# Performance work log

Hardware: AMD Instinct MI355X
Metric: run time of the kernel (lower is better)

Reference implementation:

```python
import jax, jax.numpy as jnp
import numpy as np

B, S, H, KVH, D = 1, 2048, 32, 8, 128
ROPE_THETA = 500000.0


def _rotate_half(x):
    x1, x2 = jnp.split(x, 2, axis=-1)
    return jnp.concatenate((-x2, x1), axis=-1)


def setup_inputs() -> dict:
    key = jax.random.key(0)
    ks = jax.random.split(key, 5)
    hidden_states = jax.random.normal(ks[0], (B, S, H * D), dtype=jnp.float32)
    Wq = jax.random.normal(ks[1], (H * D, H * D), dtype=jnp.float32) * 0.02
    Wk = jax.random.normal(ks[2], (KVH * D, H * D), dtype=jnp.float32) * 0.02
    Wv = jax.random.normal(ks[3], (KVH * D, H * D), dtype=jnp.float32) * 0.02
    Wo = jax.random.normal(ks[4], (H * D, H * D), dtype=jnp.float32) * 0.02
    # rotary tables (Llama-style, concat of freqs with itself)
    inv_freq = 1.0 / (ROPE_THETA ** (jnp.arange(0, D, 2, dtype=jnp.float32) / D))
    freqs = jnp.arange(S, dtype=jnp.float32)[:, None] * inv_freq[None, :]  # [S, D/2]
    emb = jnp.concatenate((freqs, freqs), axis=-1)  # [S, D]
    cos = jnp.cos(emb)[None]  # [1, S, D]
    sin = jnp.sin(emb)[None]
    # additive causal mask, matching SDPA attn_mask semantics
    causal = jnp.tril(jnp.ones((S, S), dtype=bool))
    attention_mask = jnp.where(causal, 0.0, -1e9).astype(jnp.float32)[None, None]  # [1,1,S,S]
    return {"hidden_states": hidden_states, "attention_mask": attention_mask,
            "cos": cos, "sin": sin, "Wq": Wq, "Wk": Wk, "Wv": Wv, "Wo": Wo}


def reference(hidden_states, attention_mask, cos, sin, Wq, Wk, Wv, Wo):
    b, s, _ = hidden_states.shape
    d = cos.shape[-1]
    h = Wq.shape[0] // d
    kvh = Wk.shape[0] // d
    g = h // kvh  # GQA group size

    # fused QKV projection (nn.Linear: y = x @ W^T), then split heads -> [b, heads, s, d]
    q = jnp.einsum('bsi,oi->bso', hidden_states, Wq).reshape(b, s, h, d).transpose(0, 2, 1, 3)
    k = jnp.einsum('bsi,oi->bso', hidden_states, Wk).reshape(b, s, kvh, d).transpose(0, 2, 1, 3)
    v = jnp.einsum('bsi,oi->bso', hidden_states, Wv).reshape(b, s, kvh, d).transpose(0, 2, 1, 3)

    # rotary embedding (unsqueeze_dim=1)
    c = cos[:, None]  # [b,1,s,d]
    sn = sin[:, None]
    q = q * c + _rotate_half(q) * sn
    k = k * c + _rotate_half(k) * sn

    # GQA: view q as [b, kvh, g, s, d]; contract against un-repeated k/v
    qg = q.reshape(b, kvh, g, s, d)
    scale = 1.0 / jnp.sqrt(jnp.float32(d))
    scores = jnp.einsum('bkgsd,bktd->bkgst', qg, k) * scale  # [b,kvh,g,s,s]
    scores = scores + attention_mask[:, :, None]  # broadcast [b,1,1,s,s]
    probs = jax.nn.softmax(scores, axis=-1)
    attn = jnp.einsum('bkgst,bktd->bkgsd', probs, v)  # [b,kvh,g,s,d]

    attn = attn.reshape(b, h, s, d).transpose(0, 2, 1, 3).reshape(b, s, h * d)
    out = jnp.einsum('bso,po->bsp', attn, Wo)
    return out
```

## Files before the change

### kernel.cpp

```cpp
#include <hip/hip_runtime.h>
#include <hip/hip_bf16.h>

#define SEQ 2048
#define HD  128
#define NH  32
#define NKV 8
#define MODEL 4096
#define KVDIM 1024
#define QKVN 6144

typedef __attribute__((ext_vector_type(8))) short short8;
typedef __attribute__((ext_vector_type(4))) short short4v;
typedef __attribute__((ext_vector_type(4))) float float4v;

#define MFMA16(a, b, c) __builtin_amdgcn_mfma_f32_16x16x32_bf16(a, b, c, 0, 0, 0)

__device__ __forceinline__ short f2bf(float x) {
  unsigned u = __builtin_bit_cast(unsigned, x);
  u += 0x7fffu + ((u >> 16) & 1u);
  return (short)(u >> 16);
}

__device__ __forceinline__ void async_copy16(const void* g, void* l) {
  __builtin_amdgcn_global_load_lds((const __attribute__((address_space(1))) void*)g,
                                   (__attribute__((address_space(3))) void*)l, 16, 0, 0);
}

__global__ __launch_bounds__(256) void cast_bf16(const float* __restrict__ in,
                                                 short* __restrict__ out, int n) {
  int i = (blockIdx.x * 256 + threadIdx.x) * 4;
  if (i < n) {
    float4v v = *(const float4v*)(in + i);
    short4v o;
    o[0] = f2bf(v[0]); o[1] = f2bf(v[1]); o[2] = f2bf(v[2]); o[3] = f2bf(v[3]);
    *(short4v*)(out + i) = o;
  }
}

#define BM 128
#define BN 128
#define BK 32

__global__ __launch_bounds__(256) void gemm_nt(const short* __restrict__ A,
                                               const short* __restrict__ B,
                                               float* __restrict__ C,
                                               int M, int N, int K) {
  __shared__ __align__(16) short As[2][BM * BK];
  __shared__ __align__(16) short Bs[2][BN * BK];
  int t = threadIdx.x;
  int w = t >> 6, lane = t & 63;
  int col = lane & 15, quad = lane >> 4;
  int m0 = blockIdx.y * BM, n0 = blockIdx.x * BN;
  int wr = (w >> 1) * 64, wc = (w & 1) * 64;

  int srow   = lane >> 2;
  int schunk = (lane & 3) ^ ((lane >> 3) & 3);
  const short* Ag0 = A + (size_t)(m0 + w * 32 + srow) * K + schunk * 8;
  const short* Ag1 = Ag0 + (size_t)16 * K;
  const short* Bg0 = B + (size_t)(n0 + w * 32 + srow) * K + schunk * 8;
  const short* Bg1 = Bg0 + (size_t)16 * K;
  const int wofs0 = (w * 32) * BK;
  const int wofs1 = (w * 32 + 16) * BK;

  int aswz = (quad ^ ((col >> 1) & 3)) * 8;

  float4v acc[4][4] = {};

  async_copy16(Ag0, &As[0][wofs0]);
  async_copy16(Ag1, &As[0][wofs1]);
  async_copy16(Bg0, &Bs[0][wofs0]);
  async_copy16(Bg1, &Bs[0][wofs1]);
  __syncthreads();

  const int iters = K / BK;
  for (int it = 0; it < iters; it++) {
    const int cb = it & 1, nb = cb ^ 1;
    if (it + 1 < iters) {
      const int k0 = (it + 1) * BK;
      async_copy16(Ag0 + k0, &As[nb][wofs0]);
      async_copy16(Ag1 + k0, &As[nb][wofs1]);
      async_copy16(Bg0 + k0, &Bs[nb][wofs0]);
      async_copy16(Bg1 + k0, &Bs[nb][wofs1]);
    }
    short8 af[4], bfr[4];
#pragma unroll
    for (int i = 0; i < 4; i++)
      af[i] = *(const short8*)&As[cb][(wr + i * 16 + col) * BK + aswz];
#pragma unroll
    for (int i = 0; i < 4; i++)
      bfr[i] = *(const short8*)&Bs[cb][(wc + i * 16 + col) * BK + aswz];
#pragma unroll
    for (int mi = 0; mi < 4; mi++)
#pragma unroll
      for (int ni = 0; ni < 4; ni++)
        acc[mi][ni] = MFMA16(af[mi], bfr[ni], acc[mi][ni]);
    __syncthreads();
  }

#pragma unroll
  for (int mi = 0; mi < 4; mi++)
#pragma unroll
    for (int ni = 0; ni < 4; ni++)
#pragma unroll
      for (int r = 0; r < 4; r++) {
        int row = m0 + wr + mi * 16 + quad * 4 + r;
        int cc  = n0 + wc + ni * 16 + col;
        C[(size_t)row * N + cc] = acc[mi][ni][r];
      }
}

__global__ __launch_bounds__(128) void rope_kernel(const float* __restrict__ qkv,
                                                   const float* __restrict__ cosp,
                                                   const float* __restrict__ sinp,
                                                   short* __restrict__ qb,
                                                   short* __restrict__ kb) {
  int s = blockIdx.x, head = blockIdx.y, d = threadIdx.x;
  float c  = cosp[s * HD + d];
  float sn = sinp[s * HD + d];
  if (head < NH) {
    const float* base = qkv + (size_t)s * QKVN + head * HD;
    float x = base[d];
    float rot = (d < 64) ? -base[d + 64] : base[d - 64];
    qb[((size_t)(head * SEQ + s)) * HD + d] = f2bf((x * c + rot * sn) * 0.08838834764831845f);
  } else {
    int hk = head - NH;
    const float* base = qkv + (size_t)s * QKVN + MODEL + hk * HD;
    float x = base[d];
    float rot = (d < 64) ? -base[d + 64] : base[d - 64];
    kb[((size_t)(hk * SEQ + s)) * HD + d] = f2bf(x * c + rot * sn);
  }
}

__global__ __launch_bounds__(256) void vtrans_kernel(const float* __restrict__ qkv,
                                                     short* __restrict__ vt) {
  __shared__ float tile[32][33];
  int kv = blockIdx.z;
  int d0 = blockIdx.x * 32, s0 = blockIdx.y * 32;
  int tx = threadIdx.x, ty = threadIdx.y;
#pragma unroll
  for (int j = 0; j < 32; j += 8)
    tile[ty + j][tx] = qkv[(size_t)(s0 + ty + j) * QKVN + MODEL + KVDIM + kv * HD + d0 + tx];
  __syncthreads();
#pragma unroll
  for (int j = 0; j < 32; j += 8)
    vt[((size_t)(kv * HD + d0 + ty + j)) * SEQ + s0 + tx] = f2bf(tile[tx][ty + j]);
}

#define FKT 32
#define KLD 136
#define VLD 40
#define PLD 40

__global__ __launch_bounds__(256, 3) void flash_attn(const short* __restrict__ qb_,
                                                     const short* __restrict__ kb,
                                                     const short* __restrict__ vt,
                                                     short* __restrict__ attn) {
  __shared__ __align__(16) short Ks[2][FKT * KLD];
  __shared__ __align__(16) short Vs[2][HD * VLD];
  __shared__ __align__(16) short Ps[4][32 * PLD];
  const int tid = threadIdx.x;
  const int w = tid >> 6, lane = tid & 63;
  const int col = lane & 15, quad = lane >> 4;
  const int h = blockIdx.x;
  const int kv = h >> 2;
  const int yp = (blockIdx.y < 8) ? (15 - (int)blockIdx.y) : ((int)blockIdx.y - 8);
  const int qB0 = yp * 128;
  const int q0w = qB0 + w * 32;
  const int ntiles = qB0 / FKT + 4;

  short8 ones;
#pragma unroll
  for (int i = 0; i < 8; i++) ones[i] = (short)0x3F80;

  short8 qf[2][4];
  const short* qbase = qb_ + ((size_t)(h * SEQ + q0w + col)) * HD;
#pragma unroll
  for (int rt = 0; rt < 2; rt++)
#pragma unroll
    for (int ks = 0; ks < 4; ks++)
      qf[rt][ks] = *(const short8*)(qbase + rt * 16 * HD + ks * 32 + quad * 8);

  float4v o[2][8] = {};
  float4v la[2] = {};

  const int kg_off = tid * 8;
  const int klds0  = (kg_off >> 7) * KLD + (kg_off & 127);
  const int vd     = tid >> 2;
  const int vkof   = (tid & 3) * 8;
  const size_t vrow0 = ((size_t)(kv * HD + vd)) * SEQ;
  const size_t vrow1 = ((size_t)(kv * HD + vd + 64)) * SEQ;
  const int vlds0 = vd * VLD + vkof;
  const short* kgbase = kb + ((size_t)kv * SEQ) * HD;

  short8 kr0, kr1, vr0, vr1;
  kr0 = *(const short8*)(kgbase + kg_off);
  kr1 = *(const short8*)(kgbase + 2048 + kg_off);
  vr0 = *(const short8*)(vt + vrow0 + vkof);
  vr1 = *(const short8*)(vt + vrow1 + vkof);
  *(short8*)&Ks[0][klds0]            = kr0;
  *(short8*)&Ks[0][klds0 + 16 * KLD] = kr1;
  *(short8*)&Vs[0][vlds0]            = vr0;
  *(short8*)&Vs[0][vlds0 + 64 * VLD] = vr1;
  __syncthreads();

  for (int kt = 0; kt < ntiles; kt++) {
    const int b = kt & 1;
    const int key0 = kt * FKT;
    if (kt + 1 < ntiles) {
      const int nk0 = key0 + FKT;
      const short* kg = kgbase + (size_t)nk0 * HD;
      kr0 = *(const short8*)(kg + kg_off);
      kr1 = *(const short8*)(kg + 2048 + kg_off);
      vr0 = *(const short8*)(vt + vrow0 + nk0 + vkof);
      vr1 = *(const short8*)(vt + vrow1 + nk0 + vkof);
    }
    if (key0 <= q0w + 31) {
      float4v sc[2][2] = {};
#pragma unroll
      for (int ks = 0; ks < 4; ks++) {
        short8 kf0 = *(const short8*)&Ks[b][col * KLD + ks * 32 + quad * 8];
        short8 kf1 = *(const short8*)&Ks[b][(16 + col) * KLD + ks * 32 + quad * 8];
        sc[0][0] = MFMA16(qf[0][ks], kf0, sc[0][0]);
        sc[0][1] = MFMA16(qf[0][ks], kf1, sc[0][1]);
        sc[1][0] = MFMA16(qf[1][ks], kf0, sc[1][0]);
        sc[1][1] = MFMA16(qf[1][ks], kf1, sc[1][1]);
      }
      short* pw = Ps[w];
#pragma unroll
      for (int rt = 0; rt < 2; rt++)
#pragma unroll
        for (int r = 0; r < 4; r++) {
          int row = q0w + rt * 16 + quad * 4 + r;
          float s0 = sc[rt][0][r]; if (key0 + col > row)      s0 = -INFINITY;
          float s1 = sc[rt][1][r]; if (key0 + 16 + col > row) s1 = -INFINITY;
          pw[(rt * 16 + quad * 4 + r) * PLD + col]      = f2bf(__expf(s0));
          pw[(rt * 16 + quad * 4 + r) * PLD + 16 + col] = f2bf(__expf(s1));
        }
      asm volatile("s_waitcnt lgkmcnt(0)" ::: "memory");
      short8 pf0 = *(const short8*)&pw[col * PLD + quad * 8];
      short8 pf1 = *(const short8*)&pw[(16 + col) * PLD + quad * 8];
      la[0] = MFMA16(pf0, ones, la[0]);
      la[1] = MFMA16(pf1, ones, la[1]);
#pragma unroll
      for (int nc = 0; nc < 8; nc++) {
        short8 vb = *(const short8*)&Vs[b][(nc * 16 + col) * VLD + quad * 8];
        o[0][nc] = MFMA16(pf0, vb, o[0][nc]);
        o[1][nc] = MFMA16(pf1, vb, o[1][nc]);
      }
    }
    if (kt + 1 < ntiles) {
      const int nb = 1 - b;
      *(short8*)&Ks[nb][klds0]            = kr0;
      *(short8*)&Ks[nb][klds0 + 16 * KLD] = kr1;
      *(short8*)&Vs[nb][vlds0]            = vr0;
      *(short8*)&Vs[nb][vlds0 + 64 * VLD] = vr1;
    }
    __syncthreads();
  }

  float inv[2][4];
#pragma unroll
  for (int rt = 0; rt < 2; rt++)
#pragma unroll
    for (int r = 0; r < 4; r++) inv[rt][r] = 1.0f / la[rt][r];
#pragma unroll
  for (int rt = 0; rt < 2; rt++)
#pragma unroll
    for (int nc = 0; nc < 8; nc++)
#pragma unroll
      for (int r = 0; r < 4; r++) {
        int row = q0w + rt * 16 + quad * 4 + r;
        attn[(size_t)row * MODEL + h * HD + nc * 16 + col] = f2bf(o[rt][nc][r] * inv[rt][r]);
      }
}

extern "C" void kernel_launch(void* const* d_in, const int* in_sizes, int n_in,
                              void* d_out, int out_size, void* d_ws, size_t ws_size,
                              hipStream_t stream) {
  const float* hidden = (const float*)d_in[0];
  const float* cosp = (const float*)d_in[2];
  const float* sinp = (const float*)d_in[3];
  const float* Wq   = (const float*)d_in[4];
  const float* Wk   = (const float*)d_in[5];
  const float* Wv   = (const float*)d_in[6];
  const float* Wo   = (const float*)d_in[7];

  char* ws = (char*)d_ws;
  size_t off = 0;
  auto alloc = [&](size_t bytes) {
    char* p = ws + off;
    off += (bytes + 255) & ~(size_t)255;
    return p;
  };
  short* wq_bf = (short*)alloc((size_t)MODEL * MODEL * 2);
  short* wk_bf = (short*)alloc((size_t)KVDIM * MODEL * 2);
  short* wv_bf = (short*)alloc((size_t)KVDIM * MODEL * 2);
  short* wo_bf = (short*)alloc((size_t)MODEL * MODEL * 2);
  short* h_bf  = (short*)alloc((size_t)SEQ * MODEL * 2);
  float* qkv_f32 = (float*)alloc((size_t)SEQ * QKVN * 4);
  short* k_bf  = (short*)alloc((size_t)NKV * SEQ * HD * 2);
  short* v_t   = (short*)alloc((size_t)NKV * HD * SEQ * 2);
  short* q_bf    = h_bf;
  short* attn_bf = (short*)qkv_f32;

  {
    int n;
    n = SEQ * MODEL;    cast_bf16<<<n / 1024, 256, 0, stream>>>(hidden, h_bf, n);
    n = MODEL * MODEL;  cast_bf16<<<n / 1024, 256, 0, stream>>>(Wq, wq_bf, n);
    n = KVDIM * MODEL;  cast_bf16<<<n / 1024, 256, 0, stream>>>(Wk, wk_bf, n);
    n = KVDIM * MODEL;  cast_bf16<<<n / 1024, 256, 0, stream>>>(Wv, wv_bf, n);
    n = MODEL * MODEL;  cast_bf16<<<n / 1024, 256, 0, stream>>>(Wo, wo_bf, n);
  }

  gemm_nt<<<dim3(QKVN / BN, SEQ / BM), 256, 0, stream>>>(h_bf, wq_bf, qkv_f32, SEQ, QKVN, MODEL);

  rope_kernel<<<dim3(SEQ, NH + NKV), 128, 0, stream>>>(qkv_f32, cosp, sinp, q_bf, k_bf);
  vtrans_kernel<<<dim3(HD / 32, SEQ / 32, NKV), dim3(32, 8), 0, stream>>>(qkv_f32, v_t);

  flash_attn<<<dim3(NH, SEQ / 128), 256, 0, stream>>>(q_bf, k_bf, v_t, attn_bf);

  gemm_nt<<<dim3(MODEL / BN, SEQ / BM), 256, 0, stream>>>(attn_bf, wo_bf, (float*)d_out, SEQ, MODEL, MODEL);
}
```

Baseline: 529.2 us.

## Store QKV projection in bf16 and transpose flash-attention score MFMAs for vectorized stores

The QKV GEMM now writes bf16 instead of fp32 through a templated store, which halves the intermediate traffic read by the rope and V-transpose kernels. In flash attention the score and PV MFMAs swap operands so each lane holds consecutive keys or output columns. This allows packed short4 writes of P into shared memory and vectorized output stores. Rounding Q/K/V to bf16 before RoPE adds a small extra precision loss.

```diff
diff --git a/kernel.cpp b/kernel.cpp
--- a/kernel.cpp
+++ b/kernel.cpp
@@ -19,6 +19,10 @@
   unsigned u = __builtin_bit_cast(unsigned, x);
   u += 0x7fffu + ((u >> 16) & 1u);
   return (short)(u >> 16);
+}
+__device__ __forceinline__ float bf2f(short s) {
+  unsigned u = ((unsigned)(unsigned short)s) << 16;
+  return __builtin_bit_cast(float, u);
 }
 
 __device__ __forceinline__ void async_copy16(const void* g, void* l) {
@@ -41,9 +45,13 @@
 #define BN 128
 #define BK 32
 
+__device__ __forceinline__ void store_out(float* C, size_t idx, float v) { C[idx] = v; }
+__device__ __forceinline__ void store_out(short* C, size_t idx, float v) { C[idx] = f2bf(v); }
+
+template <typename OUT>
 __global__ __launch_bounds__(256) void gemm_nt(const short* __restrict__ A,
                                                const short* __restrict__ B,
-                                               float* __restrict__ C,
+                                               OUT* __restrict__ C,
                                                int M, int N, int K) {
   __shared__ __align__(16) short As[2][BM * BK];
   __shared__ __align__(16) short Bs[2][BN * BK];
@@ -105,11 +113,11 @@
       for (int r = 0; r < 4; r++) {
         int row = m0 + wr + mi * 16 + quad * 4 + r;
         int cc  = n0 + wc + ni * 16 + col;
-        C[(size_t)row * N + cc] = acc[mi][ni][r];
+        store_out(C, (size_t)row * N + cc, acc[mi][ni][r]);
       }
 }
 
-__global__ __launch_bounds__(128) void rope_kernel(const float* __restrict__ qkv,
+__global__ __launch_bounds__(128) void rope_kernel(const short* __restrict__ qkv,
                                                    const float* __restrict__ cosp,
                                                    const float* __restrict__ sinp,
                                                    short* __restrict__ qb,
@@ -118,22 +126,22 @@
   float c  = cosp[s * HD + d];
   float sn = sinp[s * HD + d];
   if (head < NH) {
-    const float* base = qkv + (size_t)s * QKVN + head * HD;
-    float x = base[d];
-    float rot = (d < 64) ? -base[d + 64] : base[d - 64];
+    const short* base = qkv + (size_t)s * QKVN + head * HD;
+    float x = bf2f(base[d]);
+    float rot = (d < 64) ? -bf2f(base[d + 64]) : bf2f(base[d - 64]);
     qb[((size_t)(head * SEQ + s)) * HD + d] = f2bf((x * c + rot * sn) * 0.08838834764831845f);
   } else {
     int hk = head - NH;
-    const float* base = qkv + (size_t)s * QKVN + MODEL + hk * HD;
-    float x = base[d];
-    float rot = (d < 64) ? -base[d + 64] : base[d - 64];
+    const short* base = qkv + (size_t)s * QKVN + MODEL + hk * HD;
+    float x = bf2f(base[d]);
+    float rot = (d < 64) ? -bf2f(base[d + 64]) : bf2f(base[d - 64]);
     kb[((size_t)(hk * SEQ + s)) * HD + d] = f2bf(x * c + rot * sn);
   }
 }
 
-__global__ __launch_bounds__(256) void vtrans_kernel(const float* __restrict__ qkv,
+__global__ __launch_bounds__(256) void vtrans_kernel(const short* __restrict__ qkv,
                                                      short* __restrict__ vt) {
-  __shared__ float tile[32][33];
+  __shared__ short tile[32][34];
   int kv = blockIdx.z;
   int d0 = blockIdx.x * 32, s0 = blockIdx.y * 32;
   int tx = threadIdx.x, ty = threadIdx.y;
@@ -143,7 +151,7 @@
   __syncthreads();
 #pragma unroll
   for (int j = 0; j < 32; j += 8)
-    vt[((size_t)(kv * HD + d0 + ty + j)) * SEQ + s0 + tx] = f2bf(tile[tx][ty + j]);
+    vt[((size_t)(kv * HD + d0 + ty + j)) * SEQ + s0 + tx] = tile[tx][ty + j];
 }
 
 #define FKT 32
@@ -215,37 +223,43 @@
       vr1 = *(const short8*)(vt + vrow1 + nk0 + vkof);
     }
     if (key0 <= q0w + 31) {
-      float4v sc[2][2] = {};
+      float4v sct[2][2] = {};
 #pragma unroll
       for (int ks = 0; ks < 4; ks++) {
         short8 kf0 = *(const short8*)&Ks[b][col * KLD + ks * 32 + quad * 8];
         short8 kf1 = *(const short8*)&Ks[b][(16 + col) * KLD + ks * 32 + quad * 8];
-        sc[0][0] = MFMA16(qf[0][ks], kf0, sc[0][0]);
-        sc[0][1] = MFMA16(qf[0][ks], kf1, sc[0][1]);
-        sc[1][0] = MFMA16(qf[1][ks], kf0, sc[1][0]);
-        sc[1][1] = MFMA16(qf[1][ks], kf1, sc[1][1]);
+        sct[0][0] = MFMA16(kf0, qf[0][ks], sct[0][0]);
+        sct[0][1] = MFMA16(kf0, qf[1][ks], sct[0][1]);
+        sct[1][0] = MFMA16(kf1, qf[0][ks], sct[1][0]);
+        sct[1][1] = MFMA16(kf1, qf[1][ks], sct[1][1]);
       }
       short* pw = Ps[w];
 #pragma unroll
-      for (int rt = 0; rt < 2; rt++)
-#pragma unroll
-        for (int r = 0; r < 4; r++) {
-          int row = q0w + rt * 16 + quad * 4 + r;
-          float s0 = sc[rt][0][r]; if (key0 + col > row)      s0 = -INFINITY;
-          float s1 = sc[rt][1][r]; if (key0 + 16 + col > row) s1 = -INFINITY;
-          pw[(rt * 16 + quad * 4 + r) * PLD + col]      = f2bf(__expf(s0));
-          pw[(rt * 16 + quad * 4 + r) * PLD + 16 + col] = f2bf(__expf(s1));
+      for (int rt = 0; rt < 2; rt++) {
+        int qrow = q0w + rt * 16 + col;
+#pragma unroll
+        for (int kt2 = 0; kt2 < 2; kt2++) {
+          int keyb = key0 + kt2 * 16 + quad * 4;
+          short4v p;
+#pragma unroll
+          for (int r = 0; r < 4; r++) {
+            float s = sct[kt2][rt][r];
+            if (keyb + r > qrow) s = -INFINITY;
+            p[r] = f2bf(__expf(s));
+          }
+          *(short4v*)&pw[(rt * 16 + col) * PLD + kt2 * 16 + quad * 4] = p;
         }
+      }
       asm volatile("s_waitcnt lgkmcnt(0)" ::: "memory");
       short8 pf0 = *(const short8*)&pw[col * PLD + quad * 8];
       short8 pf1 = *(const short8*)&pw[(16 + col) * PLD + quad * 8];
-      la[0] = MFMA16(pf0, ones, la[0]);
-      la[1] = MFMA16(pf1, ones, la[1]);
+      la[0] = MFMA16(ones, pf0, la[0]);
+      la[1] = MFMA16(ones, pf1, la[1]);
 #pragma unroll
       for (int nc = 0; nc < 8; nc++) {
         short8 vb = *(const short8*)&Vs[b][(nc * 16 + col) * VLD + quad * 8];
-        o[0][nc] = MFMA16(pf0, vb, o[0][nc]);
-        o[1][nc] = MFMA16(pf1, vb, o[1][nc]);
+        o[0][nc] = MFMA16(vb, pf0, o[0][nc]);
+        o[1][nc] = MFMA16(vb, pf1, o[1][nc]);
       }
     }
     if (kt + 1 < ntiles) {
@@ -258,20 +272,18 @@
     __syncthreads();
   }
 
-  float inv[2][4];
-#pragma unroll
-  for (int rt = 0; rt < 2; rt++)
-#pragma unroll
-    for (int r = 0; r < 4; r++) inv[rt][r] = 1.0f / la[rt][r];
-#pragma unroll
-  for (int rt = 0; rt < 2; rt++)
-#pragma unroll
-    for (int nc = 0; nc < 8; nc++)
-#pragma unroll
-      for (int r = 0; r < 4; r++) {
-        int row = q0w + rt * 16 + quad * 4 + r;
-        attn[(size_t)row * MODEL + h * HD + nc * 16 + col] = f2bf(o[rt][nc][r] * inv[rt][r]);
-      }
+#pragma unroll
+  for (int rt = 0; rt < 2; rt++) {
+    float inv = 1.0f / la[rt][0];
+    size_t rowbase = (size_t)(q0w + rt * 16 + col) * MODEL + h * HD + quad * 4;
+#pragma unroll
+    for (int nc = 0; nc < 8; nc++) {
+      short4v ov;
+#pragma unroll
+      for (int r = 0; r < 4; r++) ov[r] = f2bf(o[rt][nc][r] * inv);
+      *(short4v*)(attn + rowbase + nc * 16) = ov;
+    }
+  }
 }
 
 extern "C" void kernel_launch(void* const* d_in, const int* in_sizes, int n_in,
@@ -297,11 +309,11 @@
   short* wv_bf = (short*)alloc((size_t)KVDIM * MODEL * 2);
   short* wo_bf = (short*)alloc((size_t)MODEL * MODEL * 2);
   short* h_bf  = (short*)alloc((size_t)SEQ * MODEL * 2);
-  float* qkv_f32 = (float*)alloc((size_t)SEQ * QKVN * 4);
+  short* qkv_bf = (short*)alloc((size_t)SEQ * QKVN * 2);
   short* k_bf  = (short*)alloc((size_t)NKV * SEQ * HD * 2);
   short* v_t   = (short*)alloc((size_t)NKV * HD * SEQ * 2);
+  short* attn_bf = (short*)alloc((size_t)SEQ * MODEL * 2);
   short* q_bf    = h_bf;
-  short* attn_bf = (short*)qkv_f32;
 
   {
     int n;
@@ -312,12 +324,12 @@
     n = MODEL * MODEL;  cast_bf16<<<n / 1024, 256, 0, stream>>>(Wo, wo_bf, n);
   }
 
-  gemm_nt<<<dim3(QKVN / BN, SEQ / BM), 256, 0, stream>>>(h_bf, wq_bf, qkv_f32, SEQ, QKVN, MODEL);
-
-  rope_kernel<<<dim3(SEQ, NH + NKV), 128, 0, stream>>>(qkv_f32, cosp, sinp, q_bf, k_bf);
-  vtrans_kernel<<<dim3(HD / 32, SEQ / 32, NKV), dim3(32, 8), 0, stream>>>(qkv_f32, v_t);
+  gemm_nt<short><<<dim3(QKVN / BN, SEQ / BM), 256, 0, stream>>>(h_bf, wq_bf, qkv_bf, SEQ, QKVN, MODEL);
+
+  rope_kernel<<<dim3(SEQ, NH + NKV), 128, 0, stream>>>(qkv_bf, cosp, sinp, q_bf, k_bf);
+  vtrans_kernel<<<dim3(HD / 32, SEQ / 32, NKV), dim3(32, 8), 0, stream>>>(qkv_bf, v_t);
 
   flash_attn<<<dim3(NH, SEQ / 128), 256, 0, stream>>>(q_bf, k_bf, v_t, attn_bf);
 
-  gemm_nt<<<dim3(MODEL / BN, SEQ / BM), 256, 0, stream>>>(attn_bf, wo_bf, (float*)d_out, SEQ, MODEL, MODEL);
-}
+  gemm_nt<float><<<dim3(MODEL / BN, SEQ / BM), 256, 0, stream>>>(attn_bf, wo_bf, (float*)d_out, SEQ, MODEL, MODEL);
+}
```

New measurement: 524.3 us. About the same (-0.9%).
